# Optimization experiments

Measured on AMD Instinct MI355X. Metric: run time of the kernel, lower is better.

Reference implementation:

```python
import jax, jax.numpy as jnp
import numpy as np

WINDOW_SIZE = 5
CONSISTENCY_WEIGHT = 1.0


def _wsum(x, w):
    # sliding-window sum along axis 1 via exclusive cumsum differences
    s = jnp.cumsum(x, axis=1)
    s = jnp.pad(s, ((0, 0), (1, 0)))
    return s[:, w:] - s[:, :-w]  # [B, L-w+1]


def setup_inputs() -> dict:
    key = jax.random.key(0)
    k1, k2, k3 = jax.random.split(key, 3)
    B, L, C = 512, 16384, 2
    return {
        "predictions": jax.random.normal(k1, (B, L, C), dtype=jnp.float32),
        "targets": jax.random.randint(k2, (B, L), 0, 2, dtype=jnp.int32),
        "mask": jax.random.randint(k3, (B, L), 0, 2, dtype=jnp.int32),
    }


def reference(predictions, targets, mask):
    w = WINDOW_SIZE
    probs = jax.nn.softmax(predictions, axis=-1)[..., 1]  # [B, L]
    t = targets.astype(jnp.float32)
    m = mask.astype(jnp.float32)

    msum = _wsum(m, w)                       # [B, W]
    denom = jnp.maximum(msum, 1.0)           # clamp(min=1.0)
    spm = _wsum(probs * m, w)
    stm = _wsum(t * m, w)
    sp2m = _wsum(probs * probs * m, w)
    st2m = _wsum(t * t * m, w)

    pmean = spm / denom
    tmean = stm / denom
    # masked biased variance: sum((x - mean)^2 * m) / clamp(msum, 1)
    pvar = (sp2m - 2.0 * pmean * spm + pmean * pmean * msum) / denom
    tvar = (st2m - 2.0 * tmean * stm + tmean * tmean * msum) / denom

    mse = jnp.mean((pvar - tvar) ** 2, axis=0)          # per-window MSE over batch, [W]
    valid = (jnp.sum(msum, axis=0) > 0).astype(jnp.float32)  # skip windows with zero mask
    cnt = jnp.maximum(jnp.sum(valid), 1.0)
    loss = jnp.sum(mse * valid) / cnt * CONSISTENCY_WEIGHT
    return loss
```

## Files before the change

kernel.cpp:

```cpp
#include <hip/hip_runtime.h>
#include <math.h>

#define BATCH 512
#define LEN   16384
#define WIN   5
#define WOUT  (LEN - WIN + 1)
#define TPB   256
#define TILE  256
#define ELEMS (TILE + WIN - 1)

__global__ void bcl_partial_kernel(const float* __restrict__ pred,
                                   const int*   __restrict__ tgt,
                                   const int*   __restrict__ msk,
                                   float* __restrict__ part_d2,
                                   float* __restrict__ part_ms,
                                   int bper) {
    __shared__ float s_m[ELEMS], s_tm[ELEMS], s_pm[ELEMS], s_p2m[ELEMS];

    const int tile0 = blockIdx.x * TILE;
    const int j     = tile0 + threadIdx.x;
    const int b0    = blockIdx.y * bper;

    float accd2 = 0.f, accms = 0.f;

    for (int b = b0; b < b0 + bper; ++b) {
        __syncthreads();
        for (int i = threadIdx.x; i < ELEMS; i += TPB) {
            const int e = tile0 + i;
            float m = 0.f, tmf = 0.f, p = 0.f;
            if (e < LEN) {
                const size_t base = (size_t)b * LEN + e;
                const int    mi = msk[base];
                const int    ti = tgt[base];
                const float2 p2 = ((const float2*)pred)[base];
                p   = 1.0f / (1.0f + __expf(p2.x - p2.y));
                m   = (float)mi;
                tmf = (float)(ti & mi);
            }
            s_m[i]   = m;
            s_tm[i]  = tmf;
            s_pm[i]  = p * m;
            s_p2m[i] = p * p * m;
        }
        __syncthreads();
        if (j < WOUT) {
            float msum = 0.f, stm = 0.f, spm = 0.f, sp2m = 0.f;
#pragma unroll
            for (int k = 0; k < WIN; ++k) {
                const int i = threadIdx.x + k;
                msum += s_m[i];
                stm  += s_tm[i];
                spm  += s_pm[i];
                sp2m += s_p2m[i];
            }
            const float denom = fmaxf(msum, 1.0f);
            const float inv   = 1.0f / denom;
            const float pmean = spm * inv;
            const float tmean = stm * inv;
            const float pvar  = (sp2m - 2.0f * pmean * spm + pmean * pmean * msum) * inv;
            const float tvar  = (stm  - 2.0f * tmean * stm + tmean * tmean * msum) * inv;
            const float d = pvar - tvar;
            accd2 += d * d;
            accms += msum;
        }
    }
    if (j < WOUT) {
        part_d2[(size_t)blockIdx.y * WOUT + j] = accd2;
        part_ms[(size_t)blockIdx.y * WOUT + j] = accms;
    }
}

__global__ void bcl_window_reduce(const float* __restrict__ part_d2,
                                  const float* __restrict__ part_ms,
                                  double* __restrict__ accum,
                                  unsigned int* __restrict__ ticket,
                                  float* __restrict__ out,
                                  int nchunks) {
    const int j = blockIdx.x * blockDim.x + threadIdx.x;
    double num = 0.0, cnt = 0.0;
    if (j < WOUT) {
        float d2 = 0.f, ms = 0.f;
        for (int c = 0; c < nchunks; ++c) {
            d2 += part_d2[(size_t)c * WOUT + j];
            ms += part_ms[(size_t)c * WOUT + j];
        }
        if (ms > 0.f) {
            num = (double)d2 * (1.0 / (double)BATCH);
            cnt = 1.0;
        }
    }
    for (int off = 32; off > 0; off >>= 1) {
        num += __shfl_down(num, off, 64);
        cnt += __shfl_down(cnt, off, 64);
    }
    __shared__ double s_num[4], s_cnt[4];
    const int lane = threadIdx.x & 63, wave = threadIdx.x >> 6;
    if (lane == 0) { s_num[wave] = num; s_cnt[wave] = cnt; }
    __syncthreads();
    if (threadIdx.x == 0) {
        double n = 0.0, c = 0.0;
        const int nw = (int)(blockDim.x >> 6);
        for (int wv = 0; wv < nw; ++wv) { n += s_num[wv]; c += s_cnt[wv]; }
        atomicAdd(&accum[0], n);
        atomicAdd(&accum[1], c);
        __threadfence();
        const unsigned int t = atomicAdd(ticket, 1u);
        if (t == gridDim.x - 1) {
            out[0] = (float)(accum[0] / fmax(accum[1], 1.0));
        }
    }
}

extern "C" void kernel_launch(void* const* d_in, const int* in_sizes, int n_in,
                              void* d_out, int out_size, void* d_ws, size_t ws_size,
                              hipStream_t stream) {
    const float* pred = (const float*)d_in[0];
    const int*   tgt  = (const int*)d_in[1];
    const int*   msk  = (const int*)d_in[2];
    float* out = (float*)d_out;

    int nchunks = 32;
    while (nchunks > 1) {
        size_t need = (size_t)nchunks * WOUT * 2 * sizeof(float) + 64;
        if (need <= ws_size) break;
        nchunks >>= 1;
    }
    const int bper = BATCH / nchunks;

    float* part_d2 = (float*)d_ws;
    float* part_ms = part_d2 + (size_t)nchunks * WOUT;
    size_t off = ((size_t)nchunks * WOUT * 2 * sizeof(float) + 15) & ~(size_t)15;
    double* accum = (double*)((char*)d_ws + off);
    unsigned int* ticket = (unsigned int*)(accum + 2);

    hipMemsetAsync((void*)accum, 0, 2 * sizeof(double) + sizeof(unsigned int), stream);

    const int WBLKS = (WOUT + TILE - 1) / TILE;

    dim3 g1(WBLKS, nchunks);
    bcl_partial_kernel<<<g1, TPB, 0, stream>>>(pred, tgt, msk, part_d2, part_ms, bper);

    bcl_window_reduce<<<WBLKS, TPB, 0, stream>>>(part_d2, part_ms, accum, ticket, out, nchunks);
}
```

Baseline: 169.5 us.

## Register-tile four windows per thread with vectorized loads, dropping shared memory

Each thread now computes four adjacent sliding windows. It loads its eight-element span with int4/float4 vector loads and keeps the per-element terms in registers, replacing the shared-memory tile and the two barriers per batch row. Partial results are written with float4 stores. The batch is split into more chunks for parallelism, and the reduce kernel gets its own fixed launch geometry. The cost is that neighbouring threads load overlapping halves of the same data and redo its exp, so global/cache traffic and transcendental work roughly double.

```diff
diff --git a/kernel.cpp b/kernel.cpp
--- a/kernel.cpp
+++ b/kernel.cpp
@@ -5,53 +5,65 @@
 #define LEN   16384
 #define WIN   5
 #define WOUT  (LEN - WIN + 1)
-#define TPB   256
-#define TILE  256
-#define ELEMS (TILE + WIN - 1)
+#define TPB   128
+#define WPT   4
+#define WPB   (TPB * WPT)
+#define EPT   (WPT + WIN - 1)
 
-__global__ void bcl_partial_kernel(const float* __restrict__ pred,
-                                   const int*   __restrict__ tgt,
-                                   const int*   __restrict__ msk,
-                                   float* __restrict__ part_d2,
-                                   float* __restrict__ part_ms,
-                                   int bper) {
-    __shared__ float s_m[ELEMS], s_tm[ELEMS], s_pm[ELEMS], s_p2m[ELEMS];
+__global__ __launch_bounds__(TPB)
+void bcl_partial_kernel(const float* __restrict__ pred,
+                        const int*   __restrict__ tgt,
+                        const int*   __restrict__ msk,
+                        float* __restrict__ part_d2,
+                        float* __restrict__ part_ms,
+                        int bper) {
+    const int j0 = blockIdx.x * WPB + (int)threadIdx.x * WPT;
+    if (j0 >= WOUT) return;
+    const int b0 = blockIdx.y * bper;
 
-    const int tile0 = blockIdx.x * TILE;
-    const int j     = tile0 + threadIdx.x;
-    const int b0    = blockIdx.y * bper;
-
-    float accd2 = 0.f, accms = 0.f;
+    float accd2[WPT] = {0.f, 0.f, 0.f, 0.f};
+    float accms[WPT] = {0.f, 0.f, 0.f, 0.f};
 
     for (int b = b0; b < b0 + bper; ++b) {
-        __syncthreads();
-        for (int i = threadIdx.x; i < ELEMS; i += TPB) {
-            const int e = tile0 + i;
-            float m = 0.f, tmf = 0.f, p = 0.f;
-            if (e < LEN) {
-                const size_t base = (size_t)b * LEN + e;
-                const int    mi = msk[base];
-                const int    ti = tgt[base];
-                const float2 p2 = ((const float2*)pred)[base];
-                p   = 1.0f / (1.0f + __expf(p2.x - p2.y));
-                m   = (float)mi;
-                tmf = (float)(ti & mi);
+        const size_t base = (size_t)b * LEN + j0;
+
+        const int4 m0 = *(const int4*)(msk + base);
+        const int4 m1 = *(const int4*)(msk + base + 4);
+        const int4 t0 = *(const int4*)(tgt + base);
+        const int4 t1 = *(const int4*)(tgt + base + 4);
+        const float4 q0 = *(const float4*)(pred + base * 2);
+        const float4 q1 = *(const float4*)(pred + base * 2 + 4);
+        const float4 q2 = *(const float4*)(pred + base * 2 + 8);
+        const float4 q3 = *(const float4*)(pred + base * 2 + 12);
+
+        float m[EPT], tm[EPT], pm[EPT], p2m[EPT];
+        {
+            const int mi[EPT] = {m0.x, m0.y, m0.z, m0.w, m1.x, m1.y, m1.z, m1.w};
+            const int ti[EPT] = {t0.x, t0.y, t0.z, t0.w, t1.x, t1.y, t1.z, t1.w};
+            const float dx[EPT] = {q0.x - q0.y, q0.z - q0.w,
+                                   q1.x - q1.y, q1.z - q1.w,
+                                   q2.x - q2.y, q2.z - q2.w,
+                                   q3.x - q3.y, q3.z - q3.w};
+#pragma unroll
+            for (int i = 0; i < EPT; ++i) {
+                const float p  = 1.0f / (1.0f + __expf(dx[i]));
+                const float mf = (float)mi[i];
+                m[i]   = mf;
+                tm[i]  = (float)(ti[i] & mi[i]);
+                pm[i]  = p * mf;
+                p2m[i] = p * p * mf;
             }
-            s_m[i]   = m;
-            s_tm[i]  = tmf;
-            s_pm[i]  = p * m;
-            s_p2m[i] = p * p * m;
         }
-        __syncthreads();
-        if (j < WOUT) {
+
+#pragma unroll
+        for (int w = 0; w < WPT; ++w) {
             float msum = 0.f, stm = 0.f, spm = 0.f, sp2m = 0.f;
 #pragma unroll
             for (int k = 0; k < WIN; ++k) {
-                const int i = threadIdx.x + k;
-                msum += s_m[i];
-                stm  += s_tm[i];
-                spm  += s_pm[i];
-                sp2m += s_p2m[i];
+                msum += m[w + k];
+                stm  += tm[w + k];
+                spm  += pm[w + k];
+                sp2m += p2m[w + k];
             }
             const float denom = fmaxf(msum, 1.0f);
             const float inv   = 1.0f / denom;
@@ -60,14 +72,15 @@
             const float pvar  = (sp2m - 2.0f * pmean * spm + pmean * pmean * msum) * inv;
             const float tvar  = (stm  - 2.0f * tmean * stm + tmean * tmean * msum) * inv;
             const float d = pvar - tvar;
-            accd2 += d * d;
-            accms += msum;
+            accd2[w] += d * d;
+            accms[w] += msum;
         }
     }
-    if (j < WOUT) {
-        part_d2[(size_t)blockIdx.y * WOUT + j] = accd2;
-        part_ms[(size_t)blockIdx.y * WOUT + j] = accms;
-    }
+
+    *(float4*)(part_d2 + (size_t)blockIdx.y * WOUT + j0) =
+        make_float4(accd2[0], accd2[1], accd2[2], accd2[3]);
+    *(float4*)(part_ms + (size_t)blockIdx.y * WOUT + j0) =
+        make_float4(accms[0], accms[1], accms[2], accms[3]);
 }
 
 __global__ void bcl_window_reduce(const float* __restrict__ part_d2,
@@ -119,7 +132,7 @@
     const int*   msk  = (const int*)d_in[2];
     float* out = (float*)d_out;
 
-    int nchunks = 32;
+    int nchunks = 64;
     while (nchunks > 1) {
         size_t need = (size_t)nchunks * WOUT * 2 * sizeof(float) + 64;
         if (need <= ws_size) break;
@@ -135,10 +148,10 @@
 
     hipMemsetAsync((void*)accum, 0, 2 * sizeof(double) + sizeof(unsigned int), stream);
 
-    const int WBLKS = (WOUT + TILE - 1) / TILE;
-
+    const int WBLKS = (WOUT + WPB - 1) / WPB;
     dim3 g1(WBLKS, nchunks);
     bcl_partial_kernel<<<g1, TPB, 0, stream>>>(pred, tgt, msk, part_d2, part_ms, bper);
 
-    bcl_window_reduce<<<WBLKS, TPB, 0, stream>>>(part_d2, part_ms, accum, ticket, out, nchunks);
+    const int RBLKS = (WOUT + 255) / 256;
+    bcl_window_reduce<<<RBLKS, 256, 0, stream>>>(part_d2, part_ms, accum, ticket, out, nchunks);
 }
```

Result: slower. 177.5 us (+4.7%).
